# Optimization experiments

Hardware: AMD Instinct MI355X
Metric: run time of the kernel (lower is better)

Reference implementation:

```python
import jax, jax.numpy as jnp
import numpy as np

NEG_SLOPE = 0.2
EPS = 1e-16


def _add_self_loops(edge_index, edge_weight, N):
    # PyG add_self_loops with fill_value='mean': self-loop attr = mean of
    # incoming edge attrs per node (0 if node has no incoming edges).
    src, dst = edge_index[0], edge_index[1]
    ones = jnp.ones_like(edge_weight)
    cnt = jax.ops.segment_sum(ones, dst, num_segments=N)
    wsum = jax.ops.segment_sum(edge_weight, dst, num_segments=N)
    self_w = jnp.where(cnt > 0, wsum / jnp.maximum(cnt, 1.0), 0.0)
    loop = jnp.arange(N, dtype=src.dtype)
    return (jnp.concatenate([src, loop]), jnp.concatenate([dst, loop]),
            jnp.concatenate([edge_weight, self_w]))


def _gatv2_layer(x, src, dst, ew, Wl, Wr, att, We, bias, N):
    # x: [M, N, Din]; src/dst: [E']; ew: [E']; att: [H, C]
    M = x.shape[0]
    H, C = att.shape
    xl = (x @ Wl).reshape(M, N, H, C)   # source transform (lin_l)
    xr = (x @ Wr).reshape(M, N, H, C)   # target transform (lin_r)
    xj = xl[:, src]                      # [M, E', H, C] gather source feats
    xi = xr[:, dst]                      # [M, E', H, C] gather target feats
    ee = (ew[:, None] @ We).reshape(-1, H, C)  # [E', H, C] edge embedding
    s = jax.nn.leaky_relu(xi + xj + ee[None], NEG_SLOPE)
    logits = jnp.einsum('mehc,hc->meh', s, att)  # [M, E', H]
    # segment softmax over edges grouped by destination node
    smax = jax.vmap(lambda u: jax.ops.segment_max(u, dst, num_segments=N))(logits)
    a = jnp.exp(logits - smax[:, dst])
    denom = jax.vmap(lambda u: jax.ops.segment_sum(u, dst, num_segments=N))(a)
    alpha = a / (denom[:, dst] + EPS)
    msg = alpha[..., None] * xj          # [M, E', H, C]
    out = jax.vmap(lambda u: jax.ops.segment_sum(u, dst, num_segments=N))(msg)
    return out.reshape(M, N, H * C) + bias


def setup_inputs() -> dict:
    key = jax.random.key(0)
    ks = jax.random.split(key, 14)
    B, T, N, Din = 2, 8, 5000, 64
    E, H, OUT = 80000, 2, 128
    C = OUT // H  # 64
    g = jax.nn.initializers.glorot_uniform()
    inp = {
        'x': jax.random.normal(ks[0], (B, T, N, Din), jnp.float32),
        'edge_index': jax.random.randint(ks[1], (2, E), 0, N, jnp.int32),
        'edge_weight': jax.random.uniform(ks[2], (E,), jnp.float32),
        # conv1 params
        'Wl1': g(ks[3], (Din, H * C), jnp.float32),
        'Wr1': g(ks[4], (Din, H * C), jnp.float32),
        'att1': g(ks[5], (H, C), jnp.float32),
        'We1': g(ks[6], (1, H * C), jnp.float32),
        'b1': jnp.zeros((H * C,), jnp.float32),
        # conv2 params
        'Wl2': g(ks[7], (OUT, H * C), jnp.float32),
        'Wr2': g(ks[8], (OUT, H * C), jnp.float32),
        'att2': g(ks[9], (H, C), jnp.float32),
        'We2': g(ks[10], (1, H * C), jnp.float32),
        'b2': jnp.zeros((H * C,), jnp.float32),
    }
    return inp


def reference(x, edge_index, edge_weight, Wl1, Wr1, att1, We1, b1,
              Wl2, Wr2, att2, We2, b2):
    B, T, N, Din = x.shape
    M = B * T
    # Tiling edges by B*T with node offsets is equivalent to sharing the same
    # edge list across M independent graph copies -> vectorize over M.
    src, dst, ew = _add_self_loops(edge_index, edge_weight, N)
    h = x.reshape(M, N, Din)
    h = _gatv2_layer(h, src, dst, ew, Wl1, Wr1, att1, We1, b1, N)
    h = jax.nn.elu(h)
    h = _gatv2_layer(h, src, dst, ew, Wl2, Wr2, att2, We2, b2, N)
    h = jax.nn.elu(h)
    return h.reshape(B, T, N, -1)
```

## Files before the change

kernel.cpp:

```cpp
#include <hip/hip_runtime.h>
#include <cstdint>
#include <cstddef>

static constexpr float NEG_SLOPE_C = 0.2f;
static constexpr float EPS_C = 1e-16f;
static constexpr float LOG2E_C = 1.4426950408889634f;
static constexpr float QA_C = 0.6f * LOG2E_C;
static constexpr float QB_C = 0.4f * LOG2E_C;

#if defined(__has_builtin)
#if __has_builtin(__builtin_amdgcn_exp2f)
#define EXP2F(x) __builtin_amdgcn_exp2f(x)
#else
#define EXP2F(x) exp2f(x)
#endif
#else
#define EXP2F(x) exp2f(x)
#endif

typedef __attribute__((ext_vector_type(8))) short bf16x8;
typedef __attribute__((ext_vector_type(4))) float f32x4;
typedef __attribute__((ext_vector_type(2))) float f32x2;

__device__ __forceinline__ short bf16_rne(float x) {
    unsigned u = __float_as_uint(x);
    u = (u + 0x7FFF + ((u >> 16) & 1)) >> 16;
    return (short)u;
}
__device__ __forceinline__ float bf16f(short s) {
    return __uint_as_float(((unsigned)(unsigned short)s) << 16);
}

template<int CTRL>
__device__ __forceinline__ float dpp_add_f(float v) {
    int x = __builtin_amdgcn_update_dpp(0, __float_as_int(v), CTRL, 0xf, 0xf, true);
    return v + __int_as_float(x);
}

__device__ __forceinline__ float reduce8(float q) {
    q = dpp_add_f<0xB1>(q);
    q = dpp_add_f<0x4E>(q);
    q = dpp_add_f<0x141>(q);
    return q;
}

struct v8 { f32x2 h[4]; };
__device__ __forceinline__ v8 load8(const float4* base, int idx) {
    v8 r;
    const float4 a = base[idx];
    const float4 b = base[idx + 1];
    r.h[0] = (f32x2){a.x, a.y}; r.h[1] = (f32x2){a.z, a.w};
    r.h[2] = (f32x2){b.x, b.y}; r.h[3] = (f32x2){b.z, b.w};
    return r;
}


__global__ void degree_kernel(const int* __restrict__ ei, const float* __restrict__ ew,
                              int E, int* __restrict__ cnt, float* __restrict__ wsum) {
    int e = blockIdx.x * blockDim.x + threadIdx.x;
    if (e >= E) return;
    int dst = ei[E + e];
    atomicAdd(&cnt[dst], 1);
    atomicAdd(&wsum[dst], ew[e]);
}

__global__ void scan_kernel(const int* __restrict__ cnt, const float* __restrict__ wsum,
                            int N, int E, int* __restrict__ offs, float* __restrict__ self_w) {
    __shared__ int bufA[1024];
    __shared__ int bufB[1024];
    int t = threadIdx.x;
    int chunk = (N + 1023) / 1024;
    int lo = t * chunk;
    int hi = lo + chunk; if (hi > N) hi = N; if (lo > N) lo = N;
    int s = 0;
    for (int n = lo; n < hi; ++n) s += cnt[n];
    bufA[t] = s;
    __syncthreads();
    int* srcb = bufA; int* dstb = bufB;
    for (int d = 1; d < 1024; d <<= 1) {
        int v = srcb[t];
        if (t >= d) v += srcb[t - d];
        dstb[t] = v;
        __syncthreads();
        int* tmp = srcb; srcb = dstb; dstb = tmp;
    }
    int run = (t == 0) ? 0 : srcb[t - 1];
    for (int n = lo; n < hi; ++n) { offs[n] = run; run += cnt[n]; }
    if (t == 0) offs[N] = E;
    for (int n = t; n < N; n += 1024) {
        int c = cnt[n];
        self_w[n] = (c > 0) ? (wsum[n] / (float)c) : 0.0f;
    }
}

__global__ void scatter_kernel(const int* __restrict__ ei, const float* __restrict__ ew, int E,
                               const int* __restrict__ offs, int* __restrict__ cursor,
                               int2* __restrict__ pairs) {
    int e = blockIdx.x * blockDim.x + threadIdx.x;
    if (e >= E) return;
    int dst = ei[E + e];
    int pos = offs[dst] + atomicAdd(&cursor[dst], 1);
    pairs[pos] = make_int2(ei[e], __float_as_int(ew[e]));
}


template<int K>
__global__ void wprep_kernel(const float* __restrict__ Wl, const float* __restrict__ Wr,
                             uint4* __restrict__ Wf) {
    const int gid = blockIdx.x * 256 + threadIdx.x;
    const int lane = gid & 63;
    const int t = (gid >> 6) & 15;
    const int s = gid >> 10;
    const int mr = lane & 15, q = lane >> 4;
    const int col = t * 16 + mr;
    const float* src = (col < 128) ? (Wl + col) : (Wr + col - 128);
    union { short sh[8]; uint4 u; } hv, lv;
    #pragma unroll
    for (int j = 0; j < 8; ++j) {
        const float v = src[(size_t)(s * 32 + q * 8 + j) * 128];
        const short h = bf16_rne(v);
        hv.sh[j] = h;
        lv.sh[j] = bf16_rne(v - bf16f(h));
    }
    const size_t base = (size_t)s * 2048 + (size_t)(t * 2) * 64 + lane;
    Wf[base] = hv.u;
    Wf[base + 64] = lv.u;
}


template<int K>
__global__ __launch_bounds__(256) void gemm_mfma_kernel(
    const float* __restrict__ X, const uint4* __restrict__ Wf,
    float* __restrict__ outL, float* __restrict__ outR) {
    __shared__ uint4 wbuf[2048];
    const int tid = threadIdx.x;
    const int wv = tid >> 6;
    const int lane = tid & 63;
    const int q = lane >> 4;
    const int mr = lane & 15;
    const int xrow = blockIdx.x * 64 + wv * 16 + mr;

    f32x4 acc[16];
    #pragma unroll
    for (int t = 0; t < 16; ++t) acc[t] = (f32x4){0.f, 0.f, 0.f, 0.f};

    const float* xp = X + (size_t)xrow * K + q * 8;

    for (int s = 0; s < K / 32; ++s) {
        const float4 a0 = *(const float4*)(xp + s * 32);
        const float4 a1 = *(const float4*)(xp + s * 32 + 4);

        __syncthreads();
        const uint4* gsrc = Wf + (size_t)s * 2048 + wv * 512 + lane;
        #pragma unroll
        for (int i = 0; i < 8; ++i)
            wbuf[wv * 512 + i * 64 + lane] = gsrc[i * 64];
        __syncthreads();

        const float av[8] = {a0.x, a0.y, a0.z, a0.w, a1.x, a1.y, a1.z, a1.w};
        bf16x8 xh, xl;
        #pragma unroll
        for (int j = 0; j < 8; ++j) {
            const short h = bf16_rne(av[j]);
            xh[j] = h;
            xl[j] = bf16_rne(av[j] - bf16f(h));
        }
        #pragma unroll
        for (int t = 0; t < 16; ++t) {
            const bf16x8 wh = *(const bf16x8*)&wbuf[(t * 2) * 64 + lane];
            const bf16x8 wl = *(const bf16x8*)&wbuf[(t * 2 + 1) * 64 + lane];
            acc[t] = __builtin_amdgcn_mfma_f32_16x16x32_bf16(wh, xh, acc[t], 0, 0, 0);
            acc[t] = __builtin_amdgcn_mfma_f32_16x16x32_bf16(wl, xh, acc[t], 0, 0, 0);
            acc[t] = __builtin_amdgcn_mfma_f32_16x16x32_bf16(wh, xl, acc[t], 0, 0, 0);
        }
    }

    const size_t ob = (size_t)xrow * 128 + q * 4;
    #pragma unroll
    for (int t = 0; t < 8; ++t) {
        *(float4*)(outL + ob + t * 16) =
            make_float4(acc[t][0], acc[t][1], acc[t][2], acc[t][3]);
        *(float4*)(outR + ob + t * 16) =
            make_float4(acc[t + 8][0], acc[t + 8][1], acc[t + 8][2], acc[t + 8][3]);
    }
}


__global__ __launch_bounds__(256) void edge_kernel(
    const float* __restrict__ xl, const float* __restrict__ xr,
    const int* __restrict__ offs, const int2* __restrict__ pairs,
    const float* __restrict__ self_w,
    const float* __restrict__ att, const float* __restrict__ We,
    const float* __restrict__ bias, float* __restrict__ out,
    int N, int M) {
    const int wave = __builtin_amdgcn_readfirstlane(threadIdx.x >> 6);
    const int b = blockIdx.x;
    const int hb = (b >= 10000) ? (b - 10000) : b;
    const int m = ((b >= 10000) ? 8 : 0) + (hb & 7);
    const int n = (hb >> 3) * 4 + wave;
    if (n >= N) return;
    const int lane = threadIdx.x & 63;
    const int p = lane >> 4;
    const int u = lane & 15;
    const int cb = u * 2;

    const float4* xlm4 = (const float4*)(xl + (size_t)m * N * 128);
    const float4* xrm4 = (const float4*)(xr + (size_t)m * N * 128);

    const v8 attL = load8((const float4*)att, cb);
    const v8 weL  = load8((const float4*)We, cb);
    const v8 xiL  = load8(xrm4, n * 32 + cb);

    float base_, lsum;
    f32x2 acc0, acc1, acc2, acc3;
    {
        const float sw = self_w[n];
        const v8 xj = load8(xlm4, n * 32 + cb);
        const f32x2 swv = (f32x2){sw, sw};
        f32x2 qa = (f32x2){0.f, 0.f}, qb = (f32x2){0.f, 0.f};
        #pragma unroll
        for (int i = 0; i < 4; ++i) {
            const f32x2 v = __builtin_elementwise_fma(swv, weL.h[i], xiL.h[i]) + xj.h[i];
            const f32x2 av = __builtin_elementwise_abs(v);
            qa = __builtin_elementwise_fma(attL.h[i], v, qa);
            qb = __builtin_elementwise_fma(attL.h[i], av, qb);
        }
        float q = fmaf(QA_C, qa[0] + qa[1], QB_C * (qb[0] + qb[1]));
        base_ = reduce8(q);
        lsum = 0.25f;
        const f32x2 qv = (f32x2){0.25f, 0.25f};
        acc0 = xj.h[0] * qv; acc1 = xj.h[1] * qv;
        acc2 = xj.h[2] * qv; acc3 = xj.h[3] * qv;
    }

    const int beg = offs[n], end = offs[n + 1];
    for (int e0 = beg; e0 < end; e0 += 4) {
        const int idx = e0 + p;
        const bool valid = idx < end;
        const int2 pr = pairs[valid ? idx : (end - 1)];
        const int src = pr.x;
        const float w = __int_as_float(pr.y);
        const v8 xj = load8(xlm4, src * 32 + cb);
        const f32x2 wv = (f32x2){w, w};
        f32x2 qa = (f32x2){0.f, 0.f}, qb = (f32x2){0.f, 0.f};
        #pragma unroll
        for (int i = 0; i < 4; ++i) {
            const f32x2 v = __builtin_elementwise_fma(wv, weL.h[i], xiL.h[i]) + xj.h[i];
            const f32x2 av = __builtin_elementwise_abs(v);
            qa = __builtin_elementwise_fma(attL.h[i], v, qa);
            qb = __builtin_elementwise_fma(attL.h[i], av, qb);
        }
        float q = fmaf(QA_C, qa[0] + qa[1], QB_C * (qb[0] + qb[1]));
        q = reduce8(q);
        float t = EXP2F(q - base_);
        t = valid ? t : 0.f;
        lsum += t;
        const f32x2 tv = (f32x2){t, t};
        acc0 = __builtin_elementwise_fma(tv, xj.h[0], acc0);
        acc1 = __builtin_elementwise_fma(tv, xj.h[1], acc1);
        acc2 = __builtin_elementwise_fma(tv, xj.h[2], acc2);
        acc3 = __builtin_elementwise_fma(tv, xj.h[3], acc3);
    }

    lsum += __shfl_xor(lsum, 16, 64);
    lsum += __shfl_xor(lsum, 32, 64);
    #define CMB(a) \
        a[0] += __shfl_xor(a[0], 16, 64); a[0] += __shfl_xor(a[0], 32, 64); \
        a[1] += __shfl_xor(a[1], 16, 64); a[1] += __shfl_xor(a[1], 32, 64)
    CMB(acc0); CMB(acc1); CMB(acc2); CMB(acc3);
    #undef CMB

    if (p == 0) {
        const float inv = 1.f / (lsum + EPS_C);
        const v8 bi = load8((const float4*)bias, cb);
        const f32x2 iv = (f32x2){inv, inv};
        f32x2 o0 = __builtin_elementwise_fma(acc0, iv, bi.h[0]);
        f32x2 o1 = __builtin_elementwise_fma(acc1, iv, bi.h[1]);
        f32x2 o2 = __builtin_elementwise_fma(acc2, iv, bi.h[2]);
        f32x2 o3 = __builtin_elementwise_fma(acc3, iv, bi.h[3]);
        float o[8] = {o0[0], o0[1], o1[0], o1[1], o2[0], o2[1], o3[0], o3[1]};
        #pragma unroll
        for (int i = 0; i < 8; ++i) o[i] = o[i] > 0.f ? o[i] : (__expf(o[i]) - 1.f);
        float4* ob = (float4*)(out + (size_t)m * N * 128);
        ob[n * 32 + cb]     = make_float4(o[0], o[1], o[2], o[3]);
        ob[n * 32 + cb + 1] = make_float4(o[4], o[5], o[6], o[7]);
    }
}


extern "C" void kernel_launch(void* const* d_in, const int* in_sizes, int n_in,
                              void* d_out, int out_size, void* d_ws, size_t ws_size,
                              hipStream_t stream) {
    const float* x    = (const float*)d_in[0];
    const int*   ei   = (const int*)d_in[1];
    const float* ew   = (const float*)d_in[2];
    const float* Wl1  = (const float*)d_in[3];
    const float* Wr1  = (const float*)d_in[4];
    const float* att1 = (const float*)d_in[5];
    const float* We1  = (const float*)d_in[6];
    const float* b1   = (const float*)d_in[7];
    const float* Wl2  = (const float*)d_in[8];
    const float* Wr2  = (const float*)d_in[9];
    const float* att2 = (const float*)d_in[10];
    const float* We2  = (const float*)d_in[11];
    const float* b2   = (const float*)d_in[12];

    const int E = in_sizes[1] / 2;
    const int N = 5000;
    const int R = out_size / 128;
    const int M = R / N;

    char* ws = (char*)d_ws;
    size_t off = 0;
    auto alloc = [&](size_t bytes) {
        char* p = ws + off;
        off = (off + bytes + 255) & ~(size_t)255;
        return p;
    };
    int*   cnt    = (int*)  alloc((size_t)3 * N * 4);
    float* wsum   = (float*)(cnt + N);
    int*   cursor = cnt + 2 * N;
    float* selfw  = (float*)alloc((size_t)N * 4);
    int*   offs   = (int*)  alloc((size_t)(N + 1) * 4);
    int2*  pairs  = (int2*) alloc((size_t)E * 8);
    uint4* wf1    = (uint4*)alloc((size_t)2 * 2048 * 16);
    uint4* wf2    = (uint4*)alloc((size_t)4 * 2048 * 16);
    float* bufA   = (float*)alloc((size_t)R * 128 * 4);
    float* bufB   = (float*)alloc((size_t)R * 128 * 4);
    float* bufC   = (float*)alloc((size_t)R * 128 * 4);

    hipMemsetAsync(cnt, 0, (size_t)3 * N * 4, stream);

    int eb = (E + 255) / 256;
    degree_kernel<<<eb, 256, 0, stream>>>(ei, ew, E, cnt, wsum);
    scan_kernel<<<1, 1024, 0, stream>>>(cnt, wsum, N, E, offs, selfw);
    scatter_kernel<<<eb, 256, 0, stream>>>(ei, ew, E, offs, cursor, pairs);
    wprep_kernel<64><<<8, 256, 0, stream>>>(Wl1, Wr1, wf1);
    wprep_kernel<128><<<16, 256, 0, stream>>>(Wl2, Wr2, wf2);

    const int gb = R / 64;
    const int tb = 2 * ((N + 3) / 4) * 8;

    gemm_mfma_kernel<64><<<gb, 256, 0, stream>>>(x, wf1, bufA, bufB);
    edge_kernel<<<tb, 256, 0, stream>>>(bufA, bufB, offs, pairs, selfw,
                                        att1, We1, b1, bufC, N, M);
    gemm_mfma_kernel<128><<<gb, 256, 0, stream>>>(bufC, wf2, bufA, bufB);
    edge_kernel<<<tb, 256, 0, stream>>>(bufA, bufB, offs, pairs, selfw,
                                        att2, We2, b2, (float*)d_out, N, M);
}
```

Measured before the change: 314.8 us.

## Process 8 edges per wave with 16 channels per lane in GATv2 edge kernel

```diff
diff --git a/kernel.cpp b/kernel.cpp
--- a/kernel.cpp
+++ b/kernel.cpp
@@ -5,8 +5,6 @@
 static constexpr float NEG_SLOPE_C = 0.2f;
 static constexpr float EPS_C = 1e-16f;
 static constexpr float LOG2E_C = 1.4426950408889634f;
-static constexpr float QA_C = 0.6f * LOG2E_C;
-static constexpr float QB_C = 0.4f * LOG2E_C;
 
 #if defined(__has_builtin)
 #if __has_builtin(__builtin_amdgcn_exp2f)
@@ -20,7 +18,6 @@
 
 typedef __attribute__((ext_vector_type(8))) short bf16x8;
 typedef __attribute__((ext_vector_type(4))) float f32x4;
-typedef __attribute__((ext_vector_type(2))) float f32x2;
 
 __device__ __forceinline__ short bf16_rne(float x) {
     unsigned u = __float_as_uint(x);
@@ -37,21 +34,10 @@
     return v + __int_as_float(x);
 }
 
-__device__ __forceinline__ float reduce8(float q) {
+__device__ __forceinline__ float reduce4(float q) {
     q = dpp_add_f<0xB1>(q);
     q = dpp_add_f<0x4E>(q);
-    q = dpp_add_f<0x141>(q);
     return q;
-}
-
-struct v8 { f32x2 h[4]; };
-__device__ __forceinline__ v8 load8(const float4* base, int idx) {
-    v8 r;
-    const float4 a = base[idx];
-    const float4 b = base[idx + 1];
-    r.h[0] = (f32x2){a.x, a.y}; r.h[1] = (f32x2){a.z, a.w};
-    r.h[2] = (f32x2){b.x, b.y}; r.h[3] = (f32x2){b.z, b.w};
-    return r;
 }
 
 
@@ -200,90 +186,116 @@
     const int n = (hb >> 3) * 4 + wave;
     if (n >= N) return;
     const int lane = threadIdx.x & 63;
-    const int p = lane >> 4;
-    const int u = lane & 15;
-    const int cb = u * 2;
+    const int p = lane >> 3;
+    const int u = lane & 7;
+    const int cb = u * 4;
 
     const float4* xlm4 = (const float4*)(xl + (size_t)m * N * 128);
     const float4* xrm4 = (const float4*)(xr + (size_t)m * N * 128);
 
-    const v8 attL = load8((const float4*)att, cb);
-    const v8 weL  = load8((const float4*)We, cb);
-    const v8 xiL  = load8(xrm4, n * 32 + cb);
+    float4 attv[4], wev[4], xiv[4];
+    #pragma unroll
+    for (int i = 0; i < 4; ++i) {
+        attv[i] = ((const float4*)att)[cb + i];
+        attv[i].x *= LOG2E_C; attv[i].y *= LOG2E_C;
+        attv[i].z *= LOG2E_C; attv[i].w *= LOG2E_C;
+        wev[i] = ((const float4*)We)[cb + i];
+        xiv[i] = xrm4[n * 32 + cb + i];
+    }
+
+    #define CH4(XI, WE, AT, XJ, W, QACC)                                   \
+        {                                                                  \
+            float s0 = fmaf(W, WE.x, XI.x) + XJ.x;                         \
+            float s1 = fmaf(W, WE.y, XI.y) + XJ.y;                         \
+            float s2 = fmaf(W, WE.z, XI.z) + XJ.z;                         \
+            float s3 = fmaf(W, WE.w, XI.w) + XJ.w;                         \
+            s0 = fmaf(NEG_SLOPE_C - 1.0f, fminf(s0, 0.f), s0);             \
+            s1 = fmaf(NEG_SLOPE_C - 1.0f, fminf(s1, 0.f), s1);             \
+            s2 = fmaf(NEG_SLOPE_C - 1.0f, fminf(s2, 0.f), s2);             \
+            s3 = fmaf(NEG_SLOPE_C - 1.0f, fminf(s3, 0.f), s3);             \
+            QACC = fmaf(s0, AT.x, QACC);                                   \
+            QACC = fmaf(s1, AT.y, QACC);                                   \
+            QACC = fmaf(s2, AT.z, QACC);                                   \
+            QACC = fmaf(s3, AT.w, QACC);                                   \
+        }
 
     float base_, lsum;
-    f32x2 acc0, acc1, acc2, acc3;
+    float4 acc[4];
     {
         const float sw = self_w[n];
-        const v8 xj = load8(xlm4, n * 32 + cb);
-        const f32x2 swv = (f32x2){sw, sw};
-        f32x2 qa = (f32x2){0.f, 0.f}, qb = (f32x2){0.f, 0.f};
-        #pragma unroll
-        for (int i = 0; i < 4; ++i) {
-            const f32x2 v = __builtin_elementwise_fma(swv, weL.h[i], xiL.h[i]) + xj.h[i];
-            const f32x2 av = __builtin_elementwise_abs(v);
-            qa = __builtin_elementwise_fma(attL.h[i], v, qa);
-            qb = __builtin_elementwise_fma(attL.h[i], av, qb);
-        }
-        float q = fmaf(QA_C, qa[0] + qa[1], QB_C * (qb[0] + qb[1]));
-        base_ = reduce8(q);
-        lsum = 0.25f;
-        const f32x2 qv = (f32x2){0.25f, 0.25f};
-        acc0 = xj.h[0] * qv; acc1 = xj.h[1] * qv;
-        acc2 = xj.h[2] * qv; acc3 = xj.h[3] * qv;
+        float4 xj[4];
+        float q0 = 0.f, q1 = 0.f, q2 = 0.f, q3 = 0.f;
+        #pragma unroll
+        for (int i = 0; i < 4; ++i) xj[i] = xlm4[n * 32 + cb + i];
+        CH4(xiv[0], wev[0], attv[0], xj[0], sw, q0);
+        CH4(xiv[1], wev[1], attv[1], xj[1], sw, q1);
+        CH4(xiv[2], wev[2], attv[2], xj[2], sw, q2);
+        CH4(xiv[3], wev[3], attv[3], xj[3], sw, q3);
+        base_ = reduce4((q0 + q1) + (q2 + q3));
+        lsum = 0.125f;
+        #pragma unroll
+        for (int i = 0; i < 4; ++i)
+            acc[i] = make_float4(xj[i].x * 0.125f, xj[i].y * 0.125f,
+                                 xj[i].z * 0.125f, xj[i].w * 0.125f);
     }
 
     const int beg = offs[n], end = offs[n + 1];
-    for (int e0 = beg; e0 < end; e0 += 4) {
+    for (int e0 = beg; e0 < end; e0 += 8) {
         const int idx = e0 + p;
         const bool valid = idx < end;
         const int2 pr = pairs[valid ? idx : (end - 1)];
         const int src = pr.x;
         const float w = __int_as_float(pr.y);
-        const v8 xj = load8(xlm4, src * 32 + cb);
-        const f32x2 wv = (f32x2){w, w};
-        f32x2 qa = (f32x2){0.f, 0.f}, qb = (f32x2){0.f, 0.f};
-        #pragma unroll
-        for (int i = 0; i < 4; ++i) {
-            const f32x2 v = __builtin_elementwise_fma(wv, weL.h[i], xiL.h[i]) + xj.h[i];
-            const f32x2 av = __builtin_elementwise_abs(v);
-            qa = __builtin_elementwise_fma(attL.h[i], v, qa);
-            qb = __builtin_elementwise_fma(attL.h[i], av, qb);
-        }
-        float q = fmaf(QA_C, qa[0] + qa[1], QB_C * (qb[0] + qb[1]));
-        q = reduce8(q);
+        float4 xj[4];
+        #pragma unroll
+        for (int i = 0; i < 4; ++i) xj[i] = xlm4[src * 32 + cb + i];
+        float q0 = 0.f, q1 = 0.f, q2 = 0.f, q3 = 0.f;
+        CH4(xiv[0], wev[0], attv[0], xj[0], w, q0);
+        CH4(xiv[1], wev[1], attv[1], xj[1], w, q1);
+        CH4(xiv[2], wev[2], attv[2], xj[2], w, q2);
+        CH4(xiv[3], wev[3], attv[3], xj[3], w, q3);
+        const float q = reduce4((q0 + q1) + (q2 + q3));
         float t = EXP2F(q - base_);
         t = valid ? t : 0.f;
         lsum += t;
-        const f32x2 tv = (f32x2){t, t};
-        acc0 = __builtin_elementwise_fma(tv, xj.h[0], acc0);
-        acc1 = __builtin_elementwise_fma(tv, xj.h[1], acc1);
-        acc2 = __builtin_elementwise_fma(tv, xj.h[2], acc2);
-        acc3 = __builtin_elementwise_fma(tv, xj.h[3], acc3);
-    }
-
-    lsum += __shfl_xor(lsum, 16, 64);
-    lsum += __shfl_xor(lsum, 32, 64);
-    #define CMB(a) \
-        a[0] += __shfl_xor(a[0], 16, 64); a[0] += __shfl_xor(a[0], 32, 64); \
-        a[1] += __shfl_xor(a[1], 16, 64); a[1] += __shfl_xor(a[1], 32, 64)
-    CMB(acc0); CMB(acc1); CMB(acc2); CMB(acc3);
-    #undef CMB
+        #pragma unroll
+        for (int i = 0; i < 4; ++i) {
+            acc[i].x = fmaf(t, xj[i].x, acc[i].x);
+            acc[i].y = fmaf(t, xj[i].y, acc[i].y);
+            acc[i].z = fmaf(t, xj[i].z, acc[i].z);
+            acc[i].w = fmaf(t, xj[i].w, acc[i].w);
+        }
+    }
+    #undef CH4
+
+    #pragma unroll
+    for (int d = 8; d <= 32; d <<= 1) {
+        lsum += __shfl_xor(lsum, d, 64);
+        #pragma unroll
+        for (int i = 0; i < 4; ++i) {
+            acc[i].x += __shfl_xor(acc[i].x, d, 64);
+            acc[i].y += __shfl_xor(acc[i].y, d, 64);
+            acc[i].z += __shfl_xor(acc[i].z, d, 64);
+            acc[i].w += __shfl_xor(acc[i].w, d, 64);
+        }
+    }
 
     if (p == 0) {
         const float inv = 1.f / (lsum + EPS_C);
-        const v8 bi = load8((const float4*)bias, cb);
-        const f32x2 iv = (f32x2){inv, inv};
-        f32x2 o0 = __builtin_elementwise_fma(acc0, iv, bi.h[0]);
-        f32x2 o1 = __builtin_elementwise_fma(acc1, iv, bi.h[1]);
-        f32x2 o2 = __builtin_elementwise_fma(acc2, iv, bi.h[2]);
-        f32x2 o3 = __builtin_elementwise_fma(acc3, iv, bi.h[3]);
-        float o[8] = {o0[0], o0[1], o1[0], o1[1], o2[0], o2[1], o3[0], o3[1]};
-        #pragma unroll
-        for (int i = 0; i < 8; ++i) o[i] = o[i] > 0.f ? o[i] : (__expf(o[i]) - 1.f);
         float4* ob = (float4*)(out + (size_t)m * N * 128);
-        ob[n * 32 + cb]     = make_float4(o[0], o[1], o[2], o[3]);
-        ob[n * 32 + cb + 1] = make_float4(o[4], o[5], o[6], o[7]);
+        #pragma unroll
+        for (int i = 0; i < 4; ++i) {
+            const float4 bi = ((const float4*)bias)[cb + i];
+            float o0 = fmaf(acc[i].x, inv, bi.x);
+            float o1 = fmaf(acc[i].y, inv, bi.y);
+            float o2 = fmaf(acc[i].z, inv, bi.z);
+            float o3 = fmaf(acc[i].w, inv, bi.w);
+            o0 = o0 > 0.f ? o0 : (__expf(o0) - 1.f);
+            o1 = o1 > 0.f ? o1 : (__expf(o1) - 1.f);
+            o2 = o2 > 0.f ? o2 : (__expf(o2) - 1.f);
+            o3 = o3 > 0.f ? o3 : (__expf(o3) - 1.f);
+            ob[n * 32 + cb + i] = make_float4(o0, o1, o2, o3);
+        }
     }
 }
 
```

Result: slower. 473.2 us (+50.3%).
